# Kernel optimization log

Measured on AMD Instinct MI355X. Metric: run time of the kernel, lower is better.

Reference implementation:

```python
import jax, jax.numpy as jnp
import numpy as np

N = 50000          # nodes
E = 800000         # edges per metapath
P = 4              # metapaths
IN = 256           # in_size
D = 32 * 8         # out_size * layer_num_heads = 256
SEM_H = 128        # SemanticAttention hidden


def setup_inputs() -> dict:
    key = jax.random.key(0)
    ks = jax.random.split(key, 8)
    h = jax.random.normal(ks[0], (N, IN), dtype=jnp.float32)
    src = jax.random.randint(ks[1], (P, E), 0, N, dtype=jnp.int32)
    dst = jax.random.randint(ks[2], (P, E), 0, N, dtype=jnp.int32)
    # per-metapath GraphConv weights (Glorot-ish scale)
    W_gc = jax.random.normal(ks[3], (P, IN, D), dtype=jnp.float32) / np.sqrt(IN)
    b_gc = jnp.zeros((P, D), dtype=jnp.float32)
    # SemanticAttention: Linear(D, SEM_H) -> tanh -> Linear(SEM_H, 1, bias=False)
    W1 = jax.random.normal(ks[4], (D, SEM_H), dtype=jnp.float32) / np.sqrt(D)
    b1 = jnp.zeros((SEM_H,), dtype=jnp.float32)
    w2 = jax.random.normal(ks[5], (SEM_H,), dtype=jnp.float32) / np.sqrt(SEM_H)
    return {"h": h, "src": src, "dst": dst, "W_gc": W_gc, "b_gc": b_gc,
            "W1": W1, "b1": b1, "w2": w2}


def _graph_conv(h, src, dst, W, b):
    # DGL GraphConv with norm='both': D_dst^{-1/2} A D_src^{-1/2} (h W) + b
    ones = jnp.ones((src.shape[0],), dtype=h.dtype)
    deg_out = jnp.clip(jax.ops.segment_sum(ones, src, num_segments=N), 1.0)
    deg_in = jnp.clip(jax.ops.segment_sum(ones, dst, num_segments=N), 1.0)
    x = (h @ W) * jax.lax.rsqrt(deg_out)[:, None]          # [N, D]
    agg = jax.ops.segment_sum(x[src], dst, num_segments=N)  # gather-scatter [N, D]
    return agg * jax.lax.rsqrt(deg_in)[:, None] + b


def reference(h, src, dst, W_gc, b_gc, W1, b1, w2):
    # per-metapath GraphConv (fixed small loop over P metapaths)
    zs = [_graph_conv(h, src[p], dst[p], W_gc[p], b_gc[p]) for p in range(P)]
    z = jnp.stack(zs, axis=1)                               # [N, P, D]
    # SemanticAttention: project -> mean over nodes -> softmax over metapaths
    s = jnp.tanh(z @ W1 + b1) @ w2                          # [N, P]
    beta = jax.nn.softmax(s.mean(axis=0), axis=0)           # [P]
    return jnp.einsum('npd,p->nd', z, beta)                 # [N, D]
```

## Files before the change

### kernel.cpp

```cpp
#include <hip/hip_runtime.h>

#define NN 50000
#define NE 800000
#define NP 4
#define DIN 256
#define DD 256
#define NH 128
#define SA 40
#define NSEG 16
#define SEGE (NE / NSEG)
#define HCH 32768
#define NHC 2
#define SCH 8192
#define NSC 7
#define SPAD(k) ((k) + ((k) >> 5))

typedef __attribute__((ext_vector_type(8))) short bf16x8;
typedef __attribute__((ext_vector_type(4))) float f32x4;
typedef __attribute__((ext_vector_type(2))) float f32x2;

__device__ __forceinline__ unsigned short f2bf(float f) {
  unsigned u = __float_as_uint(f);
  u += 0x7fff + ((u >> 16) & 1);
  return (unsigned short)(u >> 16);
}
__device__ __forceinline__ float bfl(unsigned u) { return __uint_as_float(u << 16); }
__device__ __forceinline__ float bfh(unsigned u) { return __uint_as_float(u & 0xffff0000u); }


__global__ __launch_bounds__(256) void histX_kernel(const int* __restrict__ src,
                                                    const int* __restrict__ dst,
                                                    ushort* __restrict__ cntS,
                                                    ushort* __restrict__ cntD) {
  __shared__ int hs[HCH];
  int bx = blockIdx.x;
  int c = bx % NHC, s = bx / NHC;
  int p = blockIdx.y;
  const int* idx = blockIdx.z ? dst : src;
  ushort* cnt = blockIdx.z ? cntD : cntS;
  int base = c * HCH, nk = min(HCH, NN - base);
  for (int k = threadIdx.x; k < HCH; k += 256) hs[k] = 0;
  __syncthreads();
  const int4* a4 = (const int4*)(idx + (size_t)p * NE + (size_t)s * SEGE);
  for (int i = threadIdx.x; i < SEGE / 4; i += 256) {
    int4 v = a4[i];
    int k;
    k = v.x - base; if ((unsigned)k < (unsigned)nk) atomicAdd(&hs[k], 1);
    k = v.y - base; if ((unsigned)k < (unsigned)nk) atomicAdd(&hs[k], 1);
    k = v.z - base; if ((unsigned)k < (unsigned)nk) atomicAdd(&hs[k], 1);
    k = v.w - base; if ((unsigned)k < (unsigned)nk) atomicAdd(&hs[k], 1);
  }
  __syncthreads();
  ushort* out = cnt + (size_t)(p * NSEG + s) * NN + base;
  for (int k = threadIdx.x; k < nk; k += 256) out[k] = (ushort)hs[k];
}


__global__ __launch_bounds__(1024) void scanA_kernel(
    ushort* __restrict__ cntD, const ushort* __restrict__ cntS,
    float* __restrict__ rin, float* __restrict__ rout,
    int* __restrict__ row_ptr, int* __restrict__ chunkdeg) {
  int c = blockIdx.x, p = blockIdx.y;
  int base = c * SCH, nk = min(SCH, NN - base);
  __shared__ int sdeg[SCH + (SCH >> 5)];
  __shared__ int wtot[16], wexc[16];
  int t = threadIdx.x;
  for (int kk = t; kk < SCH; kk += 1024) {
    int run = 0;
    if (kk < nk) {
      size_t o = (size_t)(p * NSEG) * NN + base + kk;
      int vD[NSEG], vS[NSEG];
#pragma unroll
      for (int s = 0; s < NSEG; ++s) vD[s] = cntD[o + (size_t)s * NN];
#pragma unroll
      for (int s = 0; s < NSEG; ++s) vS[s] = cntS[o + (size_t)s * NN];
#pragma unroll
      for (int s = 0; s < NSEG; ++s) {
        cntD[o + (size_t)s * NN] = (ushort)run;
        run += vD[s];
      }
      int rs = 0;
#pragma unroll
      for (int s = 0; s < NSEG; ++s) rs += vS[s];
      rin[(size_t)p * NN + base + kk] = rsqrtf((float)max(run, 1));
      rout[(size_t)p * NN + base + kk] = rsqrtf((float)max(rs, 1));
    }
    sdeg[SPAD(kk)] = run;
  }
  __syncthreads();
  int loc[8];
  int ssum = 0;
#pragma unroll
  for (int j = 0; j < 8; ++j) { loc[j] = ssum; ssum += sdeg[SPAD(t * 8 + j)]; }
  int incl = ssum;
  int lane = t & 63, w = t >> 6;
#pragma unroll
  for (int o = 1; o < 64; o <<= 1) {
    int v = __shfl_up(incl, o);
    if (lane >= o) incl += v;
  }
  if (lane == 63) wtot[w] = incl;
  __syncthreads();
  if (t == 0) {
    int r = 0;
    for (int i = 0; i < 16; ++i) { wexc[i] = r; r += wtot[i]; }
  }
  __syncthreads();
  int tbase = wexc[w] + incl - ssum;
  int* rp = row_ptr + (size_t)p * (NN + 1) + base;
#pragma unroll
  for (int j = 0; j < 8; ++j) {
    int k = t * 8 + j;
    if (k < nk) rp[k] = tbase + loc[j];
  }
  if (t == 1023) chunkdeg[p * NSC + c] = tbase + ssum;
}


__global__ __launch_bounds__(1024) void rpfin_kernel(int* __restrict__ row_ptr,
                                                     const int* __restrict__ chunkdeg) {
  int k = blockIdx.x * 1024 + threadIdx.x, p = blockIdx.y;
  if (k < NN) {
    int c = k >> 13;
    int cb = 0;
    for (int i = 0; i < c; ++i) cb += chunkdeg[p * NSC + i];
    row_ptr[(size_t)p * (NN + 1) + k] += cb;
  }
  if (k == 0) row_ptr[(size_t)p * (NN + 1) + NN] = NE;
}


__global__ __launch_bounds__(256) void scatter_kernel(
    const int* __restrict__ src, const int* __restrict__ dst,
    const ushort* __restrict__ cntD, const int* __restrict__ row_ptr, int* __restrict__ col) {
  __shared__ int cur[HCH];
  int bx = blockIdx.x;
  int c = bx % NHC, s = bx / NHC;
  int p = blockIdx.y;
  int base = c * HCH, nk = min(HCH, NN - base);
  for (int k = threadIdx.x; k < nk; k += 256)
    cur[k] = row_ptr[(size_t)p * (NN + 1) + base + k] +
             cntD[(size_t)(p * NSEG + s) * NN + base + k];
  __syncthreads();
  const int4* d4 = (const int4*)(dst + (size_t)p * NE + (size_t)s * SEGE);
  const int4* s4 = (const int4*)(src + (size_t)p * NE + (size_t)s * SEGE);
  int* colp = col + (size_t)p * NE;
  for (int i = threadIdx.x; i < SEGE / 4; i += 256) {
    int4 dv = d4[i];
    int4 sv = s4[i];
    int k;
    k = dv.x - base; if ((unsigned)k < (unsigned)nk) colp[atomicAdd(&cur[k], 1)] = sv.x;
    k = dv.y - base; if ((unsigned)k < (unsigned)nk) colp[atomicAdd(&cur[k], 1)] = sv.y;
    k = dv.z - base; if ((unsigned)k < (unsigned)nk) colp[atomicAdd(&cur[k], 1)] = sv.z;
    k = dv.w - base; if ((unsigned)k < (unsigned)nk) colp[atomicAdd(&cur[k], 1)] = sv.w;
  }
}


__global__ void cvt_h_kernel(const float4* __restrict__ h4, ushort4* __restrict__ h2) {
  int i = blockIdx.x * blockDim.x + threadIdx.x;
  if (i >= NN * DIN / 4) return;
  float4 v = h4[i];
  ushort4 o;
  o.x = f2bf(v.x); o.y = f2bf(v.y); o.z = f2bf(v.z); o.w = f2bf(v.w);
  h2[i] = o;
}


__global__ __launch_bounds__(256) void agg_kernel(
    const ushort* __restrict__ h2, const int* __restrict__ col,
    const int* __restrict__ row_ptr, const float* __restrict__ rout,
    const float* __restrict__ rin, ushort* __restrict__ g, int pbase) {
  __shared__ int2 sW[4][64];
  int p = pbase + blockIdx.y;
  int v = blockIdx.x * 4 + (threadIdx.x >> 6);
  int lane = threadIdx.x & 63;
  int wv = threadIdx.x >> 6;
  const int* colp = col + (size_t)p * NE;
  const float* rop = rout + (size_t)p * NN;
  int beg = row_ptr[p * (NN + 1) + v], end = row_ptr[p * (NN + 1) + v + 1];
  const char* hb = (const char*)h2 + (size_t)lane * 8;
  f32x2 accA0 = {0.f, 0.f}, accA1 = {0.f, 0.f};
  f32x2 accB0 = {0.f, 0.f}, accB1 = {0.f, 0.f};
  for (int j0 = beg; j0 < end; j0 += 64) {
    int nw = end - j0;
    if (nw > 64) nw = 64;
    int cv = 0;
    float rv = 0.f;
    if (lane < nw) { cv = colp[j0 + lane]; rv = rop[cv]; }
    sW[wv][lane] = make_int2(cv, __float_as_int(rv));
    int nwb = (nw + 7) & ~7;
    for (int t = 0; t < nwb; t += 8) {
      int2 w[8];
#pragma unroll
      for (int q = 0; q < 8; ++q) w[q] = sW[wv][t + q];
      uint2 u[8];
#pragma unroll
      for (int q = 0; q < 8; ++q)
        u[q] = *(const uint2*)(hb + ((size_t)(unsigned)w[q].x << 9));
#pragma unroll
      for (int q = 0; q < 8; ++q) {
        float r = __int_as_float(w[q].y);
        f32x2 rr = {r, r};
        if (q & 1) {
          asm("v_pk_fma_f32 %0, %1, %2, %0" : "+v"(accB0) : "v"(rr), "v"((f32x2){bfl(u[q].x), bfh(u[q].x)}));
          asm("v_pk_fma_f32 %0, %1, %2, %0" : "+v"(accB1) : "v"(rr), "v"((f32x2){bfl(u[q].y), bfh(u[q].y)}));
        } else {
          asm("v_pk_fma_f32 %0, %1, %2, %0" : "+v"(accA0) : "v"(rr), "v"((f32x2){bfl(u[q].x), bfh(u[q].x)}));
          asm("v_pk_fma_f32 %0, %1, %2, %0" : "+v"(accA1) : "v"(rr), "v"((f32x2){bfl(u[q].y), bfh(u[q].y)}));
        }
      }
    }
  }
  float ri = rin[(size_t)p * NN + v];
  f32x2 s0 = accA0 + accB0;
  f32x2 s1 = accA1 + accB1;
  ushort4 o;
  o.x = f2bf(s0.x * ri); o.y = f2bf(s0.y * ri);
  o.z = f2bf(s1.x * ri); o.w = f2bf(s1.y * ri);
  ((ushort4*)(g + ((size_t)p * NN + v) * DIN))[lane] = o;
}


__global__ void wmulcvec_kernel(const float* __restrict__ Wgc, const float* __restrict__ bgc,
                                const float* __restrict__ W1, const float* __restrict__ b1,
                                ushort* __restrict__ Mt, float* __restrict__ cvec) {
  int p = blockIdx.y, k = blockIdx.x, j = threadIdx.x;
  if (k < DIN) {
    const float* wrow = Wgc + ((size_t)p * DIN + k) * DD;
    float s = 0.f;
    for (int d = 0; d < DD; ++d) s = fmaf(wrow[d], W1[(size_t)d * NH + j], s);
    Mt[((size_t)p * NH + j) * DIN + k] = f2bf(s);
  } else {
    const float* b = bgc + (size_t)p * DD;
    float s = b1[j];
    for (int d = 0; d < DD; ++d) s = fmaf(b[d], W1[(size_t)d * NH + j], s);
    cvec[p * NH + j] = s;
  }
}


__global__ __launch_bounds__(256) void gemm_sem(
    const ushort* __restrict__ g, const ushort* __restrict__ Mt,
    const float* __restrict__ cvec, const float* __restrict__ w2,
    float* __restrict__ ssum) {
  __shared__ ushort As[128 * SA];
  __shared__ ushort Bs[128 * SA];
  __shared__ float wsumf[4];
  const int tid = threadIdx.x;
  const int p = blockIdx.y;
  const int row0 = blockIdx.x * 128;
  const int wave = tid >> 6, lane = tid & 63;
  const int wr = wave >> 1, wc = wave & 1;
  const int srow = tid >> 2, sseg = tid & 3;
  const int fr = lane & 15, fk = (lane >> 4) * 8;
  const ushort* Ag = g + (size_t)p * NN * DIN;
  const ushort* Bg = Mt + (size_t)p * NH * DIN;
  int ar0 = row0 + srow; if (ar0 >= NN) ar0 = NN - 1;
  int ar1 = row0 + srow + 64; if (ar1 >= NN) ar1 = NN - 1;
  f32x4 acc[4][4] = {};
  for (int k2 = 0; k2 < DIN; k2 += 32) {
    uint4 av0 = *(const uint4*)(Ag + (size_t)ar0 * DIN + k2 + sseg * 8);
    uint4 av1 = *(const uint4*)(Ag + (size_t)ar1 * DIN + k2 + sseg * 8);
    uint4 bv0 = *(const uint4*)(Bg + (size_t)srow * DIN + k2 + sseg * 8);
    uint4 bv1 = *(const uint4*)(Bg + (size_t)(srow + 64) * DIN + k2 + sseg * 8);
    __syncthreads();
    *(uint4*)&As[srow * SA + sseg * 8] = av0;
    *(uint4*)&As[(srow + 64) * SA + sseg * 8] = av1;
    *(uint4*)&Bs[srow * SA + sseg * 8] = bv0;
    *(uint4*)&Bs[(srow + 64) * SA + sseg * 8] = bv1;
    __syncthreads();
    bf16x8 af[4], bfv[4];
#pragma unroll
    for (int t = 0; t < 4; ++t) {
      af[t] = *(const bf16x8*)&As[(wr * 64 + t * 16 + fr) * SA + fk];
      bfv[t] = *(const bf16x8*)&Bs[(wc * 64 + t * 16 + fr) * SA + fk];
    }
#pragma unroll
    for (int mt = 0; mt < 4; ++mt)
#pragma unroll
      for (int nt = 0; nt < 4; ++nt)
        acc[mt][nt] = __builtin_amdgcn_mfma_f32_16x16x32_bf16(af[mt], bfv[nt], acc[mt][nt], 0, 0, 0);
  }
  float s = 0.f;
#pragma unroll
  for (int nt = 0; nt < 4; ++nt) {
    int c = wc * 64 + nt * 16 + fr;
    float cc = cvec[p * NH + c];
    float ww = w2[c];
#pragma unroll
    for (int mt = 0; mt < 4; ++mt)
#pragma unroll
      for (int i = 0; i < 4; ++i) {
        int r = row0 + wr * 64 + mt * 16 + (lane >> 4) * 4 + i;
        if (r < NN) {
          float x = acc[mt][nt][i] + cc;
          x = fminf(fmaxf(x, -15.f), 15.f);
          float e = __expf(2.f * x);
          s = fmaf((e - 1.f) / (e + 1.f), ww, s);
        }
      }
  }
#pragma unroll
  for (int o = 32; o > 0; o >>= 1) s += __shfl_down(s, o);
  if (lane == 0) wsumf[wave] = s;
  __syncthreads();
  if (tid == 0) atomicAdd(&ssum[p], wsumf[0] + wsumf[1] + wsumf[2] + wsumf[3]);
}


__global__ __launch_bounds__(256) void scaleWtB_kernel(const float* __restrict__ Wgc,
                                                       const float* __restrict__ ssum,
                                                       const float* __restrict__ bgc,
                                                       ushort* __restrict__ Wt,
                                                       float* __restrict__ bout) {
  float m[NP];
  float mx = -1e30f;
#pragma unroll
  for (int p = 0; p < NP; ++p) {
    m[p] = ssum[p] * (1.f / (float)NN);
    mx = fmaxf(mx, m[p]);
  }
  float tot = 0.f;
#pragma unroll
  for (int p = 0; p < NP; ++p) { m[p] = __expf(m[p] - mx); tot += m[p]; }
  float inv = 1.f / tot;
  if (blockIdx.x == 0) {
    int d = threadIdx.x;
    float s = 0.f;
#pragma unroll
    for (int p = 0; p < NP; ++p) s = fmaf(m[p] * inv, bgc[p * DD + d], s);
    bout[d] = s;
  }
  int i = blockIdx.x * 256 + threadIdx.x;
  if (i < DD * NP * DIN) {
    int n = i >> 10;
    int pk = i & 1023;
    int p = pk >> 8, k = pk & 255;
    Wt[i] = f2bf(m[p] * inv * Wgc[((size_t)p * DIN + k) * DD + n]);
  }
}


__global__ __launch_bounds__(256) void gemm_main(
    const ushort* __restrict__ g, const ushort* __restrict__ Wt,
    const float* __restrict__ bout, float* __restrict__ out) {
  __shared__ ushort As[128 * SA];
  __shared__ ushort Bs[256 * SA];
  const int tid = threadIdx.x;
  const int row0 = blockIdx.x * 128;
  const int wave = tid >> 6, lane = tid & 63;
  const int wr = wave >> 1, wc = wave & 1;
  const int srow = tid >> 2, sseg = tid & 3;
  const int fr = lane & 15, fk = (lane >> 4) * 8;
  int ar0 = row0 + srow; if (ar0 >= NN) ar0 = NN - 1;
  int ar1 = row0 + srow + 64; if (ar1 >= NN) ar1 = NN - 1;
  f32x4 acc[4][8] = {};
  for (int p = 0; p < NP; ++p) {
    const ushort* Ag = g + (size_t)p * NN * DIN;
    for (int k2 = 0; k2 < DIN; k2 += 32) {
      uint4 av0 = *(const uint4*)(Ag + (size_t)ar0 * DIN + k2 + sseg * 8);
      uint4 av1 = *(const uint4*)(Ag + (size_t)ar1 * DIN + k2 + sseg * 8);
      uint4 bv0 = *(const uint4*)(Wt + (size_t)srow * (NP * DIN) + p * DIN + k2 + sseg * 8);
      uint4 bv1 = *(const uint4*)(Wt + (size_t)(srow + 64) * (NP * DIN) + p * DIN + k2 + sseg * 8);
      uint4 bv2 = *(const uint4*)(Wt + (size_t)(srow + 128) * (NP * DIN) + p * DIN + k2 + sseg * 8);
      uint4 bv3 = *(const uint4*)(Wt + (size_t)(srow + 192) * (NP * DIN) + p * DIN + k2 + sseg * 8);
      __syncthreads();
      *(uint4*)&As[srow * SA + sseg * 8] = av0;
      *(uint4*)&As[(srow + 64) * SA + sseg * 8] = av1;
      *(uint4*)&Bs[srow * SA + sseg * 8] = bv0;
      *(uint4*)&Bs[(srow + 64) * SA + sseg * 8] = bv1;
      *(uint4*)&Bs[(srow + 128) * SA + sseg * 8] = bv2;
      *(uint4*)&Bs[(srow + 192) * SA + sseg * 8] = bv3;
      __syncthreads();
      bf16x8 af[4], bfv[8];
#pragma unroll
      for (int t = 0; t < 4; ++t)
        af[t] = *(const bf16x8*)&As[(wr * 64 + t * 16 + fr) * SA + fk];
#pragma unroll
      for (int nt = 0; nt < 8; ++nt)
        bfv[nt] = *(const bf16x8*)&Bs[(wc * 128 + nt * 16 + fr) * SA + fk];
#pragma unroll
      for (int mt = 0; mt < 4; ++mt)
#pragma unroll
        for (int nt = 0; nt < 8; ++nt)
          acc[mt][nt] = __builtin_amdgcn_mfma_f32_16x16x32_bf16(af[mt], bfv[nt], acc[mt][nt], 0, 0, 0);
    }
  }
#pragma unroll
  for (int nt = 0; nt < 8; ++nt) {
    int c = wc * 128 + nt * 16 + fr;
    float bb = bout[c];
#pragma unroll
    for (int mt = 0; mt < 4; ++mt)
#pragma unroll
      for (int i = 0; i < 4; ++i) {
        int r = row0 + wr * 64 + mt * 16 + (lane >> 4) * 4 + i;
        if (r < NN) out[(size_t)r * DD + c] = acc[mt][nt][i] + bb;
      }
  }
}


extern "C" void kernel_launch(void* const* d_in, const int* in_sizes, int n_in,
                              void* d_out, int out_size, void* d_ws, size_t ws_size,
                              hipStream_t stream) {
  const float* h = (const float*)d_in[0];
  const int* src = (const int*)d_in[1];
  const int* dst = (const int*)d_in[2];
  const float* Wgc = (const float*)d_in[3];
  const float* bgc = (const float*)d_in[4];
  const float* W1 = (const float*)d_in[5];
  const float* b1 = (const float*)d_in[6];
  const float* w2 = (const float*)d_in[7];
  float* out = (float*)d_out;

  char* base = (char*)d_ws;
  size_t off = 0;
  auto alloc = [&](size_t bytes) -> char* {
    char* ptr = base + off;
    off = (off + bytes + 255) & ~(size_t)255;
    return ptr;
  };
  ushort* cntD = (ushort*)alloc((size_t)NP * NSEG * NN * sizeof(ushort));
  ushort* cntS = (ushort*)alloc((size_t)NP * NSEG * NN * sizeof(ushort));
  float* rin = (float*)alloc((size_t)NP * NN * sizeof(float));
  float* rout = (float*)alloc((size_t)NP * NN * sizeof(float));
  int* row_ptr = (int*)alloc((size_t)NP * (NN + 1) * sizeof(int));
  int* chunkdeg = (int*)alloc((size_t)NP * NSC * sizeof(int));
  int* colbuf = (int*)alloc((size_t)NP * NE * sizeof(int));
  ushort* h2 = (ushort*)alloc((size_t)NN * DIN * sizeof(ushort));
  ushort* g = (ushort*)alloc((size_t)NP * NN * DIN * sizeof(ushort));
  ushort* Mt = (ushort*)alloc((size_t)NP * NH * DIN * sizeof(ushort));
  ushort* Wt = (ushort*)alloc((size_t)DD * NP * DIN * sizeof(ushort));
  float* cvec = (float*)alloc((size_t)NP * NH * sizeof(float));
  float* ssum = (float*)alloc(NP * sizeof(float));
  float* bout = (float*)alloc(DD * sizeof(float));
  if (off > ws_size) return;

  hipMemsetAsync(ssum, 0, NP * sizeof(float), stream);

  histX_kernel<<<dim3(NHC * NSEG, NP, 2), 256, 0, stream>>>(src, dst, cntS, cntD);
  scanA_kernel<<<dim3(NSC, NP), 1024, 0, stream>>>(cntD, cntS, rin, rout, row_ptr, chunkdeg);
  rpfin_kernel<<<dim3((NN + 1023) / 1024, NP), 1024, 0, stream>>>(row_ptr, chunkdeg);
  cvt_h_kernel<<<(NN * DIN / 4 + 255) / 256, 256, 0, stream>>>((const float4*)h, (ushort4*)h2);
  scatter_kernel<<<dim3(NHC * NSEG, NP), 256, 0, stream>>>(src, dst, cntD, row_ptr, colbuf);
  agg_kernel<<<dim3(NN / 4, 2), 256, 0, stream>>>(h2, colbuf, row_ptr, rout, rin, g, 0);
  agg_kernel<<<dim3(NN / 4, 2), 256, 0, stream>>>(h2, colbuf, row_ptr, rout, rin, g, 2);
  wmulcvec_kernel<<<dim3(DIN + 1, NP), NH, 0, stream>>>(Wgc, bgc, W1, b1, Mt, cvec);
  gemm_sem<<<dim3((NN + 127) / 128, NP), 256, 0, stream>>>(g, Mt, cvec, w2, ssum);
  scaleWtB_kernel<<<(DD * NP * DIN + 255) / 256, 256, 0, stream>>>(Wgc, ssum, bgc, Wt, bout);
  gemm_main<<<dim3((NN + 127) / 128), 256, 0, stream>>>(g, Wt, bout, out);
}
```

Measured before the change: 598.9 us.

## Split gemm_main into 128-column tiles, permute LDS staging rows, merge agg launches

gemm_main now uses 128x128 output tiles over a 2D grid instead of a 128x256 tile per block. This halves the accumulator registers and LDS per block to raise occupancy, at the cost of reading the g activations twice. The shared-memory staging row mapping is permuted in both GEMMs, likely to reduce LDS bank conflicts on stores. The two agg_kernel launches are merged into one launch covering all four metapaths, which removes a launch and adds more blocks.

```diff
diff --git a/kernel.cpp b/kernel.cpp
--- a/kernel.cpp
+++ b/kernel.cpp
@@ -252,7 +252,8 @@
   const int row0 = blockIdx.x * 128;
   const int wave = tid >> 6, lane = tid & 63;
   const int wr = wave >> 1, wc = wave & 1;
-  const int srow = tid >> 2, sseg = tid & 3;
+  const int q = tid >> 2, sseg = tid & 3;
+  const int srow = ((q & 31) << 1) | (q >> 5);
   const int fr = lane & 15, fk = (lane >> 4) * 8;
   const ushort* Ag = g + (size_t)p * NN * DIN;
   const ushort* Bg = Mt + (size_t)p * NH * DIN;
@@ -346,50 +347,47 @@
     const ushort* __restrict__ g, const ushort* __restrict__ Wt,
     const float* __restrict__ bout, float* __restrict__ out) {
   __shared__ ushort As[128 * SA];
-  __shared__ ushort Bs[256 * SA];
+  __shared__ ushort Bs[128 * SA];
   const int tid = threadIdx.x;
-  const int row0 = blockIdx.x * 128;
+  const int row0 = blockIdx.y * 128;
+  const int col0 = blockIdx.x * 128;
   const int wave = tid >> 6, lane = tid & 63;
   const int wr = wave >> 1, wc = wave & 1;
-  const int srow = tid >> 2, sseg = tid & 3;
+  const int q = tid >> 2, sseg = tid & 3;
+  const int srow = ((q & 31) << 1) | (q >> 5);
   const int fr = lane & 15, fk = (lane >> 4) * 8;
   int ar0 = row0 + srow; if (ar0 >= NN) ar0 = NN - 1;
   int ar1 = row0 + srow + 64; if (ar1 >= NN) ar1 = NN - 1;
-  f32x4 acc[4][8] = {};
+  f32x4 acc[4][4] = {};
   for (int p = 0; p < NP; ++p) {
     const ushort* Ag = g + (size_t)p * NN * DIN;
     for (int k2 = 0; k2 < DIN; k2 += 32) {
       uint4 av0 = *(const uint4*)(Ag + (size_t)ar0 * DIN + k2 + sseg * 8);
       uint4 av1 = *(const uint4*)(Ag + (size_t)ar1 * DIN + k2 + sseg * 8);
-      uint4 bv0 = *(const uint4*)(Wt + (size_t)srow * (NP * DIN) + p * DIN + k2 + sseg * 8);
-      uint4 bv1 = *(const uint4*)(Wt + (size_t)(srow + 64) * (NP * DIN) + p * DIN + k2 + sseg * 8);
-      uint4 bv2 = *(const uint4*)(Wt + (size_t)(srow + 128) * (NP * DIN) + p * DIN + k2 + sseg * 8);
-      uint4 bv3 = *(const uint4*)(Wt + (size_t)(srow + 192) * (NP * DIN) + p * DIN + k2 + sseg * 8);
+      uint4 bv0 = *(const uint4*)(Wt + (size_t)(col0 + srow) * (NP * DIN) + p * DIN + k2 + sseg * 8);
+      uint4 bv1 = *(const uint4*)(Wt + (size_t)(col0 + srow + 64) * (NP * DIN) + p * DIN + k2 + sseg * 8);
       __syncthreads();
       *(uint4*)&As[srow * SA + sseg * 8] = av0;
       *(uint4*)&As[(srow + 64) * SA + sseg * 8] = av1;
       *(uint4*)&Bs[srow * SA + sseg * 8] = bv0;
       *(uint4*)&Bs[(srow + 64) * SA + sseg * 8] = bv1;
-      *(uint4*)&Bs[(srow + 128) * SA + sseg * 8] = bv2;
-      *(uint4*)&Bs[(srow + 192) * SA + sseg * 8] = bv3;
       __syncthreads();
-      bf16x8 af[4], bfv[8];
-#pragma unroll
-      for (int t = 0; t < 4; ++t)
+      bf16x8 af[4], bfv[4];
+#pragma unroll
+      for (int t = 0; t < 4; ++t) {
         af[t] = *(const bf16x8*)&As[(wr * 64 + t * 16 + fr) * SA + fk];
-#pragma unroll
-      for (int nt = 0; nt < 8; ++nt)
-        bfv[nt] = *(const bf16x8*)&Bs[(wc * 128 + nt * 16 + fr) * SA + fk];
+        bfv[t] = *(const bf16x8*)&Bs[(wc * 64 + t * 16 + fr) * SA + fk];
+      }
 #pragma unroll
       for (int mt = 0; mt < 4; ++mt)
 #pragma unroll
-        for (int nt = 0; nt < 8; ++nt)
+        for (int nt = 0; nt < 4; ++nt)
           acc[mt][nt] = __builtin_amdgcn_mfma_f32_16x16x32_bf16(af[mt], bfv[nt], acc[mt][nt], 0, 0, 0);
     }
   }
 #pragma unroll
-  for (int nt = 0; nt < 8; ++nt) {
-    int c = wc * 128 + nt * 16 + fr;
+  for (int nt = 0; nt < 4; ++nt) {
+    int c = col0 + wc * 64 + nt * 16 + fr;
     float bb = bout[c];
 #pragma unroll
     for (int mt = 0; mt < 4; ++mt)
@@ -445,10 +443,9 @@
   rpfin_kernel<<<dim3((NN + 1023) / 1024, NP), 1024, 0, stream>>>(row_ptr, chunkdeg);
   cvt_h_kernel<<<(NN * DIN / 4 + 255) / 256, 256, 0, stream>>>((const float4*)h, (ushort4*)h2);
   scatter_kernel<<<dim3(NHC * NSEG, NP), 256, 0, stream>>>(src, dst, cntD, row_ptr, colbuf);
-  agg_kernel<<<dim3(NN / 4, 2), 256, 0, stream>>>(h2, colbuf, row_ptr, rout, rin, g, 0);
-  agg_kernel<<<dim3(NN / 4, 2), 256, 0, stream>>>(h2, colbuf, row_ptr, rout, rin, g, 2);
+  agg_kernel<<<dim3(NN / 4, NP), 256, 0, stream>>>(h2, colbuf, row_ptr, rout, rin, g, 0);
   wmulcvec_kernel<<<dim3(DIN + 1, NP), NH, 0, stream>>>(Wgc, bgc, W1, b1, Mt, cvec);
   gemm_sem<<<dim3((NN + 127) / 128, NP), 256, 0, stream>>>(g, Mt, cvec, w2, ssum);
   scaleWtB_kernel<<<(DD * NP * DIN + 255) / 256, 256, 0, stream>>>(Wgc, ssum, bgc, Wt, bout);
-  gemm_main<<<dim3((NN + 127) / 128), 256, 0, stream>>>(g, Wt, bout, out);
-}
+  gemm_main<<<dim3(2, (NN + 127) / 128), 256, 0, stream>>>(g, Wt, bout, out);
+}
```

Measured after the change: 575.0 us. 4.0% less time.
